# Kernel tuning notes

Hardware: AMD Instinct MI355X
Metric: run time of the kernel (lower is better)

## Reference

```python
import jax, jax.numpy as jnp
from jax import lax
import numpy as np
import math

# --- static equivariant-conv basis (kernel lattice offsets) ---
K = 5          # kernel size = diameter / step
NRB = 3        # num_radial_basis
RMAX = 2.5     # diameter / 2
C0, C1 = 32, 16   # hidden irreps: 32x0e + 16x1e (4*ne scalars + 2*ne vectors, ne=8)
GATES = C1        # one 0e gate scalar per gated vector irrep

_c = np.arange(K, dtype=np.float32) - K // 2
_grid = np.stack(np.meshgrid(_c, _c, _c, indexing='ij'), -1)            # [K,K,K,3]
_norm = np.linalg.norm(_grid, axis=-1)
_mask = (_norm <= RMAX).astype(np.float32)
_ctr = np.linspace(0.0, RMAX, NRB).astype(np.float32)
_w = RMAX / (NRB - 1)
R_BASIS = jnp.asarray(np.exp(-(((_norm[..., None] - _ctr) / _w) ** 2)) * _mask[..., None])  # [K,K,K,NRB]
_safe = np.where(_norm == 0.0, 1.0, _norm)
_y1 = (math.sqrt(3.0) * _grid / _safe[..., None]).astype(np.float32)    # component-normalized l=1 SH
_y1[_norm == 0.0] = 0.0
Y1_SH = jnp.asarray(_y1)                                                # [K,K,K,3]
_levi = np.zeros((3, 3, 3), np.float32)
for _a, _b, _d in ((0, 1, 2), (1, 2, 0), (2, 0, 1)):
    _levi[_a, _b, _d] = 1.0
    _levi[_a, _d, _b] = -1.0
LEVI = jnp.asarray(_levi)


def _equiv_conv(x, ss, sv, vs, vv0, vv1):
    """Equivariant voxel conv: kernel = radial(|r|) * Y_l(r) * CG, then 3D conv.
    x: [B,D,H,W, C0 + 3*C1] -> [B,D,H,W, Cso + 3*Cvo]."""
    Cso, Cvo = ss.shape[-1], sv.shape[-1]
    Kss = jnp.einsum('xyzr,rio->xyzio', R_BASIS, ss)                      # 0e->0e via Y0
    Ksv = jnp.einsum('xyzr,rio,xyzm->xyziom', R_BASIS, sv, Y1_SH)         # 0e->1  via Y1
    Kvs = jnp.einsum('xyzr,rio,xyzm->xyzimo', R_BASIS, vs, Y1_SH) / math.sqrt(3.0)  # 1->0 (dot CG)
    Kvv0 = jnp.einsum('xyzr,rio->xyzio', R_BASIS, vv0)                    # 1->1 via Y0 (identity CG)
    Kvv1 = jnp.einsum('xyzr,rio->xyzio', R_BASIS, vv1)                    # 1->1 via Y1 (cross CG)
    E1 = jnp.einsum('xyzm,amb->xyzab', Y1_SH, LEVI) / math.sqrt(2.0)
    eye = jnp.eye(3, dtype=x.dtype)
    Kvv = (Kvv0[..., :, None, :, None] * eye[None, None, None, None, :, None, :]
           + Kvv1[..., :, None, :, None] * E1[..., None, :, None, :])     # [K,K,K,C1,3,Cvo,3]
    top = jnp.concatenate([Kss, Ksv.reshape(K, K, K, C0, 3 * Cvo)], axis=-1)
    bot = jnp.concatenate([Kvs.reshape(K, K, K, 3 * C1, Cso),
                           Kvv.reshape(K, K, K, 3 * C1, 3 * Cvo)], axis=-1)
    kern = jnp.concatenate([top, bot], axis=-2)                            # [K,K,K,Fin,Fout]
    return lax.conv_general_dilated(x, kern, (1, 1, 1), 'SAME',
                                    dimension_numbers=('NDHWC', 'DHWIO', 'NDHWC'))


def _gate(y):
    """e3nn Gate: activation on scalars, sigmoid(gates) scales the vectors."""
    s = jax.nn.relu(y[..., :C0])
    g = jax.nn.sigmoid(y[..., C0:C0 + GATES])
    v = y[..., C0 + GATES:].reshape(y.shape[:-1] + (C1, 3)) * g[..., None]
    return jnp.concatenate([s, v.reshape(y.shape[:-1] + (3 * C1,))], axis=-1)


def _up2(a, axes=(1, 2, 3)):
    for ax in axes:
        a = jnp.repeat(a, 2, axis=ax)
    return a


def _forward(x, c1_ss, c1_sv, c1_vs, c1_vv0, c1_vv1,
             c2_ss, c2_sv, c2_vs, c2_vv0, c2_vv1, w_pos, wl_s, wl_v):
    # --- ConvolutionBlock: two equivariant convs, each followed by a Gate ---
    x = _gate(_equiv_conv(x, c1_ss, c1_sv, c1_vs, c1_vv0, c1_vv1))
    x = _gate(_equiv_conv(x, c2_ss, c2_sv, c2_vs, c2_vv0, c2_vv1))
    B, Dc, Hc, Wc, _F = x.shape
    # --- _get_vectors: fine-grid offsets to (recentered) upsampled coarse centers ---
    ci = jnp.stack(jnp.meshgrid(jnp.arange(Dc), jnp.arange(Hc), jnp.arange(Wc), indexing='ij'), -1)
    centers = _up2((ci + jnp.array([Dc // 2, Hc // 2, Wc // 2]))[None], (1, 2, 3))[0].astype(jnp.float32)
    fi = jnp.stack(jnp.meshgrid(jnp.arange(2 * Dc), jnp.arange(2 * Hc), jnp.arange(2 * Wc),
                                indexing='ij'), -1).astype(jnp.float32)
    vecs = fi - centers                               # [2D,2H,2W,3]
    p = w_pos * vecs                                  # position_blocks: irreps-wise 1x1 Linear
    # --- nearest-neighbor upsample of features ---
    xu = _up2(x)                                      # [B,2D,2H,2W,F]
    S = xu[..., :C0]
    V = xu[..., C0:].reshape(xu.shape[:-1] + (C1, 3))
    # --- FullTensorProduct(features, pos embedding): per-voxel CG contractions ---
    t_s = jnp.einsum('bxyzcm,xyzm->bxyzc', V, p) / math.sqrt(3.0)          # 1x1->0
    t_v_sp = S[..., None] * p[None, :, :, :, None, :]                       # 0x1->1
    t_v_vp = jnp.cross(V, p[None, :, :, :, None, :]) / math.sqrt(2.0)       # 1x1->1
    tv = jnp.concatenate([t_v_sp, t_v_vp], axis=-2)                         # [...,C0+C1,3]
    # --- rebase_blocks_linear: irreps-wise Linear back to hidden (fan-in normalized) ---
    S_out = jnp.einsum('bxyzc,co->bxyzo', t_s, wl_s) / math.sqrt(C1)
    V_out = jnp.einsum('bxyzcm,co->bxyzom', tv, wl_v) / math.sqrt(C0 + C1)
    return jnp.concatenate([S_out, V_out.reshape(V_out.shape[:-2] + (3 * C1,))], axis=-1)


def setup_inputs() -> dict:
    key = jax.random.key(0)
    ks = jax.random.split(key, 16)
    n = jax.random.normal
    s = 0.02
    B, D = 1, 32
    FIN = C0 + 3 * C1          # 80
    CSO = C0 + GATES           # 48 output scalars (incl. gates) per conv
    return {
        'x': n(ks[0], (B, D, D, D, FIN), jnp.float32),
        'c1_ss': s * n(ks[1], (NRB, C0, CSO), jnp.float32),
        'c1_sv': s * n(ks[2], (NRB, C0, C1), jnp.float32),
        'c1_vs': s * n(ks[3], (NRB, C1, CSO), jnp.float32),
        'c1_vv0': s * n(ks[4], (NRB, C1, C1), jnp.float32),
        'c1_vv1': s * n(ks[5], (NRB, C1, C1), jnp.float32),
        'c2_ss': s * n(ks[6], (NRB, C0, CSO), jnp.float32),
        'c2_sv': s * n(ks[7], (NRB, C0, C1), jnp.float32),
        'c2_vs': s * n(ks[8], (NRB, C1, CSO), jnp.float32),
        'c2_vv0': s * n(ks[9], (NRB, C1, C1), jnp.float32),
        'c2_vv1': s * n(ks[10], (NRB, C1, C1), jnp.float32),
        'w_pos': 0.1 * n(ks[11], (), jnp.float32),
        'wl_s': n(ks[12], (C1, C0), jnp.float32),
        'wl_v': n(ks[13], (C0 + C1, C1), jnp.float32),
    }


def reference(x, c1_ss, c1_sv, c1_vs, c1_vv0, c1_vv1,
              c2_ss, c2_sv, c2_vs, c2_vv0, c2_vv1, w_pos, wl_s, wl_v):
    return _forward(x, c1_ss, c1_sv, c1_vs, c1_vv0, c1_vv1,
                    c2_ss, c2_sv, c2_vs, c2_vv0, c2_vv1, w_pos, wl_s, wl_v)
```

## Files before the change

### kernel.cpp

```cpp
#include <hip/hip_runtime.h>
#include <math.h>


typedef __attribute__((ext_vector_type(8))) short bf16x8;
typedef __attribute__((ext_vector_type(4))) float f32x4;

__device__ __forceinline__ int eps3(int a, int m, int b) {
    if (a == b || a == m || m == b) return 0;
    return ((a==0&&m==1&&b==2)||(a==1&&m==2&&b==0)||(a==2&&m==0&&b==1)) ? 1 : -1;
}

__global__ void build_tap(float* __restrict__ tap) {
    int t = threadIdx.x;
    if (t >= 125) return;
    int td = t / 25 - 2, th = (t / 5) % 5 - 2, tw = t % 5 - 2;
    int n2 = td*td + th*th + tw*tw;
    if (t == 62) {
        float* rec = tap + 40 * 16;
        rec[0] = __int_as_float(0); rec[1] = __int_as_float(0);
        for (int r = 0; r < 3; r++) {
            float tt = (0.f - 1.25f * (float)r) * 0.8f;
            rec[4 + r] = expf(-tt * tt);
        }
        return;
    }
    bool active = n2 <= 6;
    bool pos = (td > 0) || (td == 0 && th > 0) || (td == 0 && th == 0 && tw > 0);
    if (!(active && pos)) return;
    int idx = 0;
    for (int q = 0; q < t; q++) {
        int qd = q / 25 - 2, qh = (q / 5) % 5 - 2, qw = q % 5 - 2;
        int m2 = qd*qd + qh*qh + qw*qw;
        bool p = (qd > 0) || (qd == 0 && qh > 0) || (qd == 0 && qh == 0 && qw > 0);
        if (m2 <= 6 && p) idx++;
    }
    float* rec = tap + idx * 16;
    int off = td * 96 + th * 12 + tw;
    rec[0] = __int_as_float(off);
    rec[1] = __int_as_float(-off);
    float norm = sqrtf((float)n2);
    float comp[3] = {(float)td, (float)th, (float)tw};
    for (int r = 0; r < 3; r++) {
        float tt = (norm - 1.25f * (float)r) * 0.8f;
        float R = expf(-tt * tt);
        rec[4 + r] = R;
        for (int m = 0; m < 3; m++)
            rec[7 + r*3 + m] = R * 1.7320508075688772f * comp[m] / norm;
    }
}

__global__ void build_W(float* __restrict__ W,
    const float* __restrict__ ss1, const float* __restrict__ sv1,
    const float* __restrict__ vs1, const float* __restrict__ vv01, const float* __restrict__ vv11,
    const float* __restrict__ ss2, const float* __restrict__ sv2,
    const float* __restrict__ vs2, const float* __restrict__ vv02, const float* __restrict__ vv12)
{
    int idx = threadIdx.x + blockIdx.x * 256;
    if (idx >= 184320) return;
    int conv = idx / 92160;
    int rem  = idx % 92160;
    int j  = rem / 7680;
    int ci = (rem / 96) % 80;
    int co = rem % 96;
    int r = j >> 2, al = j & 3;
    const float* ss  = conv ? ss2  : ss1;
    const float* sv  = conv ? sv2  : sv1;
    const float* vs  = conv ? vs2  : vs1;
    const float* vv0 = conv ? vv02 : vv01;
    const float* vv1 = conv ? vv12 : vv11;
    float val = 0.f;
    if (ci < 32) {
        if (co < 48) { if (al == 0) val = ss[(r*32 + ci)*48 + co]; }
        else {
            int o = (co - 48) / 3, m = (co - 48) % 3;
            if (al == m + 1) val = sv[(r*32 + ci)*16 + o];
        }
    } else {
        int i = (ci - 32) / 3, a = (ci - 32) % 3;
        if (co < 48) { if (al == a + 1) val = vs[(r*16 + i)*48 + co] * 0.5773502691896258f; }
        else {
            int o = (co - 48) / 3, b = (co - 48) % 3;
            if (al == 0) { if (a == b) val = vv0[(r*16 + i)*16 + o]; }
            else {
                int e = eps3(a, al - 1, b);
                if (e) val = vv1[(r*16 + i)*16 + o] * (float)e * 0.7071067811865476f;
            }
        }
    }
    W[idx] = val;
}

__global__ void build_Wc(const float* __restrict__ W,
                         unsigned short* __restrict__ Wh, unsigned short* __restrict__ Wl)
{
    int idx = threadIdx.x + blockIdx.x * 256;
    if (idx >= 184320) return;
    int conv = idx / 92160, rem = idx % 92160;
    int co = rem / 960, kp = rem % 960;
    int c5 = kp / 192, r2 = kp % 192;
    int j = r2 / 16, ci16 = r2 % 16;
    int k = j * 80 + c5 * 16 + ci16;
    float w = W[conv * 92160 + k * 96 + co];
    unsigned int u = __float_as_uint(w);
    unsigned int hib = (u + 0x7FFFu + ((u >> 16) & 1u)) & 0xFFFF0000u;
    float res = w - __uint_as_float(hib);
    unsigned int v = __float_as_uint(res);
    unsigned int lob = (v + 0x7FFFu + ((v >> 16) & 1u)) >> 16;
    Wh[idx] = (unsigned short)(hib >> 16);
    Wl[idx] = (unsigned short)lob;
}

__device__ __forceinline__ void split8(float4 a, float4 b, bf16x8& hi, bf16x8& lo) {
    float av[8] = {a.x, a.y, a.z, a.w, b.x, b.y, b.z, b.w};
    #pragma unroll
    for (int e = 0; e < 8; e++) {
        unsigned int u = __float_as_uint(av[e]);
        hi[e] = (short)(u >> 16);
        float res = av[e] - __uint_as_float(u & 0xFFFF0000u);
        lo[e] = (short)(__float_as_uint(res) >> 16);
    }
}

__global__ __launch_bounds__(512, 2) void fused_conv(
    const float* __restrict__ xin, const unsigned short* __restrict__ Wh,
    const unsigned short* __restrict__ Wl, const float* __restrict__ tap,
    float* __restrict__ xout)
{
    __shared__ float smem[38400];
    int tid = threadIdx.x;
    int cl = tid >> 7;
    int vl = tid & 127;
    int dl = vl >> 5, hl = (vl >> 3) & 3, wl = vl & 7;
    int w8 = tid >> 6, l = tid & 63;
    int lr = l & 15, lk = l >> 4;
    int bid = blockIdx.x;
    int dt = (bid >> 5) << 2;
    int h0 = ((bid >> 2) & 7) << 2;
    int w0 = (bid & 3) << 3;

    int gof[6];
    int lof[6];
    #pragma unroll
    for (int q = 0; q < 6; q++) {
        int i = tid + q * 512;
        int sl = i / 768, rr = i - sl * 768;
        int dd = rr / 96, rm = rr - dd * 96;
        int hh = rm / 12, ww = rm - hh * 12;
        int gd = dt + dd - 2, gh = h0 + hh - 2, gw = w0 + ww - 2;
        gof[q] = (gd >= 0 && gd < 32 && gh >= 0 && gh < 32 && gw >= 0 && gw < 32)
               ? (((gd << 5) + gh) * 32 + gw) * 80 + sl * 4 : -1;
        lof[q] = sl * 3072 + rr * 4;
    }

    {
        float4 pf[6];
        #pragma unroll
        for (int q = 0; q < 6; q++)
            pf[q] = (gof[q] >= 0) ? *reinterpret_cast<const float4*>(xin + gof[q])
                                  : make_float4(0.f, 0.f, 0.f, 0.f);
        #pragma unroll
        for (int q = 0; q < 6; q++)
            *reinterpret_cast<float4*>(smem + lof[q]) = pf[q];
    }
    __syncthreads();

    const f32x4 fzero = {0.f, 0.f, 0.f, 0.f};
    f32x4 acc[6];
    #pragma unroll
    for (int nt = 0; nt < 6; nt++) acc[nt] = fzero;

    float* zcb = smem + 12288;
    const float* xp = smem + cl * 3072 + (((dl + 2) * 8 + hl + 2) * 12 + (wl + 2)) * 4;
    float* zp = zcb + vl * 204;

    for (int c5 = 0; c5 < 5; c5++) {
        float4 pf[6];
        if (c5 < 4) {
            int chof = (c5 + 1) * 16;
            #pragma unroll
            for (int q = 0; q < 6; q++)
                pf[q] = (gof[q] >= 0) ? *reinterpret_cast<const float4*>(xin + gof[q] + chof)
                                      : make_float4(0.f, 0.f, 0.f, 0.f);
        }
        {
            float az[12][4];
            #pragma unroll
            for (int j = 0; j < 12; j++)
                #pragma unroll
                for (int c = 0; c < 4; c++) az[j][c] = 0.f;
            {
                const float* rec = tap + 640;
                float4 xc = *reinterpret_cast<const float4*>(xp);
                #pragma unroll
                for (int r = 0; r < 3; r++) {
                    float R = rec[4 + r];
                    az[r*4][0] += R * xc.x; az[r*4][1] += R * xc.y;
                    az[r*4][2] += R * xc.z; az[r*4][3] += R * xc.w;
                }
            }
            for (int p = 0; p < 40; p++) {
                const float* rec = tap + p * 16;
                int op = __float_as_int(rec[0]) * 4, om = __float_as_int(rec[1]) * 4;
                float4 xa = *reinterpret_cast<const float4*>(xp + op);
                float4 xb = *reinterpret_cast<const float4*>(xp + om);
                float s[4], d[4];
                s[0] = xa.x + xb.x; s[1] = xa.y + xb.y; s[2] = xa.z + xb.z; s[3] = xa.w + xb.w;
                d[0] = xa.x - xb.x; d[1] = xa.y - xb.y; d[2] = xa.z - xb.z; d[3] = xa.w - xb.w;
                #pragma unroll
                for (int r = 0; r < 3; r++) {
                    float R = rec[4 + r];
                    #pragma unroll
                    for (int c = 0; c < 4; c++) az[r*4][c] += R * s[c];
                    #pragma unroll
                    for (int m = 0; m < 3; m++) {
                        float RY = rec[7 + r*3 + m];
                        #pragma unroll
                        for (int c = 0; c < 4; c++) az[r*4 + m + 1][c] += RY * d[c];
                    }
                }
            }
            #pragma unroll
            for (int j = 0; j < 12; j++)
                *reinterpret_cast<float4*>(zp + j * 16 + cl * 4) =
                    make_float4(az[j][0], az[j][1], az[j][2], az[j][3]);
        }
        __syncthreads();
        if (c5 < 4) {
            #pragma unroll
            for (int q = 0; q < 6; q++)
                *reinterpret_cast<float4*>(smem + lof[q]) = pf[q];
        }
        const float* ap0 = zcb + (w8 * 16 + lr) * 204 + lk * 8;
        #pragma unroll
        for (int ks = 0; ks < 6; ks++) {
            const unsigned short* bbh = Wh + lr * 960 + c5 * 192 + ks * 32 + lk * 8;
            const unsigned short* bbl = Wl + lr * 960 + c5 * 192 + ks * 32 + lk * 8;
            bf16x8 bh[6], bl[6];
            #pragma unroll
            for (int nt = 0; nt < 6; nt++) {
                bh[nt] = *reinterpret_cast<const bf16x8*>(bbh + nt * 15360);
                bl[nt] = *reinterpret_cast<const bf16x8*>(bbl + nt * 15360);
            }
            const float* ap = ap0 + ks * 32;
            bf16x8 ah, al;
            split8(*reinterpret_cast<const float4*>(ap),
                   *reinterpret_cast<const float4*>(ap + 4), ah, al);
            #pragma unroll
            for (int nt = 0; nt < 6; nt++) {
                acc[nt] = __builtin_amdgcn_mfma_f32_16x16x32_bf16(ah, bh[nt], acc[nt], 0, 0, 0);
                acc[nt] = __builtin_amdgcn_mfma_f32_16x16x32_bf16(al, bh[nt], acc[nt], 0, 0, 0);
                acc[nt] = __builtin_amdgcn_mfma_f32_16x16x32_bf16(ah, bl[nt], acc[nt], 0, 0, 0);
            }
        }
        __syncthreads();
    }

    float* y = smem;
    #pragma unroll
    for (int nt = 0; nt < 6; nt++)
        #pragma unroll
        for (int r = 0; r < 4; r++)
            y[(w8 * 16 + lk * 4 + r) * 98 + nt * 16 + lr] = acc[nt][r];
    __syncthreads();
    #pragma unroll
    for (int it = 0; it < 20; it++) {
        int idx = tid + it * 512;
        int vr = idx / 80, c = idx - vr * 80;
        int gd = dt + (vr >> 5), gh = h0 + ((vr >> 3) & 3), gw = w0 + (vr & 7);
        const float* yr = y + vr * 98;
        float val;
        if (c < 32) val = fmaxf(yr[c], 0.f);
        else {
            int q = c - 32;
            float g = 1.f / (1.f + __expf(-yr[32 + q / 3]));
            val = yr[48 + q] * g;
        }
        xout[(size_t)(((gd << 5) + gh) * 32 + gw) * 80 + c] = val;
    }
}

__global__ __launch_bounds__(256) void final_k(
    const float* __restrict__ x2, const float* __restrict__ wls,
    const float* __restrict__ wlv, const float* __restrict__ wpos,
    float* __restrict__ out)
{
    __shared__ float xv[16 * 81];
    __shared__ float coeff[16 * 161];
    __shared__ float s_wls[512];
    __shared__ float s_wlv[768];
    int t = threadIdx.x;
    int bid = blockIdx.x;
    int cw0 = (bid & 1) * 16;
    int ch  = (bid >> 1) & 31;
    int cd  = bid >> 6;
    float wp = wpos[0];
    {
        int base = ((cd * 32 + ch) * 32 + cw0) * 80;
        #pragma unroll
        for (int i = t; i < 1280; i += 256) {
            int vi = i / 80, c = i % 80;
            xv[vi * 81 + c] = x2[base + i];
        }
        for (int i = t; i < 512; i += 256) s_wls[i] = wls[i];
        for (int i = t; i < 768; i += 256) s_wlv[i] = wlv[i];
    }
    __syncthreads();
    {
        int vi = t >> 4, j = t & 15;
        const float* xp = xv + vi * 81;
        float* cf = coeff + vi * 161;
        #pragma unroll
        for (int l = 0; l < 10; l++) {
            int q = l * 16 + j;
            float sum = 0.f;
            if (q < 96) {
                int o = q / 3, m = q % 3;
                #pragma unroll
                for (int c = 0; c < 16; c++) sum += xp[32 + c * 3 + m] * s_wls[c * 32 + o];
            } else if (q < 112) {
                int o = q - 96;
                #pragma unroll
                for (int c = 0; c < 32; c++) sum += xp[c] * s_wlv[c * 16 + o];
            } else {
                int q2 = q - 112; int o = q2 / 3, m = q2 % 3;
                #pragma unroll
                for (int c = 0; c < 16; c++) sum += xp[32 + c * 3 + m] * s_wlv[(32 + c) * 16 + o];
            }
            cf[q] = sum;
        }
    }
    __syncthreads();
    const float scale = 0.14433756729740643f;
    #pragma unroll
    for (int f01 = 0; f01 < 4; f01++) {
        int fd = 2 * cd + (f01 >> 1), fh = 2 * ch + (f01 & 1);
        float p0 = wp * (float)(cd + (f01 >> 1) - 16);
        float p1 = wp * (float)(ch + (f01 & 1) - 16);
        size_t obase = (size_t)((fd * 64 + fh) * 64 + cw0 * 2) * 80;
        #pragma unroll
        for (int it = 0; it < 10; it++) {
            int idx = it * 256 + t;
            int fwl = idx / 80, c = idx - fwl * 80;
            int vi = fwl >> 1;
            float p2 = wp * (float)(cw0 + vi + (fwl & 1) - 16);
            const float* cf = coeff + vi * 161;
            float val;
            if (c < 32) {
                val = cf[c * 3] * p0 + cf[c * 3 + 1] * p1 + cf[c * 3 + 2] * p2;
            } else {
                int q = c - 32, o = q / 3, m = q - o * 3;
                float A = cf[96 + o];
                const float* w2 = cf + 112 + o * 3;
                float pm, crm;
                if (m == 0)      { pm = p0; crm = w2[1] * p2 - w2[2] * p1; }
                else if (m == 1) { pm = p1; crm = w2[2] * p0 - w2[0] * p2; }
                else             { pm = p2; crm = w2[0] * p1 - w2[1] * p0; }
                val = A * pm + crm * 0.7071067811865476f;
            }
            out[obase + idx] = val * scale;
        }
    }
}

extern "C" void kernel_launch(void* const* d_in, const int* in_sizes, int n_in,
                              void* d_out, int out_size, void* d_ws, size_t ws_size,
                              hipStream_t stream)
{
    const float* x    = (const float*)d_in[0];
    const float* wpos = (const float*)d_in[11];
    const float* wls  = (const float*)d_in[12];
    const float* wlv  = (const float*)d_in[13];
    float* out = (float*)d_out;
    float* ws  = (float*)d_ws;

    float* tap = ws;
    float* W   = ws + 1024;
    unsigned short* Wh = (unsigned short*)(ws + 1024 + 184320);
    unsigned short* Wl = Wh + 184320;
    float* x1  = ws + 1024 + 184320 + 184320;
    float* x2  = x1 + 2621440;

    build_tap<<<1, 128, 0, stream>>>(tap);
    build_W<<<720, 256, 0, stream>>>(W,
        (const float*)d_in[1], (const float*)d_in[2], (const float*)d_in[3],
        (const float*)d_in[4], (const float*)d_in[5],
        (const float*)d_in[6], (const float*)d_in[7], (const float*)d_in[8],
        (const float*)d_in[9], (const float*)d_in[10]);
    build_Wc<<<720, 256, 0, stream>>>(W, Wh, Wl);

    fused_conv<<<256, 512, 0, stream>>>(x,  Wh,         Wl,         tap, x1);
    fused_conv<<<256, 512, 0, stream>>>(x1, Wh + 92160, Wl + 92160, tap, x2);
    final_k<<<2048, 256, 0, stream>>>(x2, wls, wlv, wpos, out);
}
```

Baseline: 419.9 us.

## Double fused_conv block size to 1024 threads and vectorize final_k stores

```diff
diff --git a/kernel.cpp b/kernel.cpp
--- a/kernel.cpp
+++ b/kernel.cpp
@@ -121,28 +121,27 @@
     }
 }
 
-__global__ __launch_bounds__(512, 2) void fused_conv(
+__global__ __launch_bounds__(1024, 4) void fused_conv(
     const float* __restrict__ xin, const unsigned short* __restrict__ Wh,
     const unsigned short* __restrict__ Wl, const float* __restrict__ tap,
     float* __restrict__ xout)
 {
-    __shared__ float smem[38400];
+    __shared__ float smem[37376];
     int tid = threadIdx.x;
-    int cl = tid >> 7;
-    int vl = tid & 127;
+    int vl = tid & 127, cg = tid >> 7;
     int dl = vl >> 5, hl = (vl >> 3) & 3, wl = vl & 7;
-    int w8 = tid >> 6, l = tid & 63;
+    int w16 = tid >> 6, l = tid & 63;
     int lr = l & 15, lk = l >> 4;
+    int rt = w16 >> 1, nh = w16 & 1;
     int bid = blockIdx.x;
     int dt = (bid >> 5) << 2;
     int h0 = ((bid >> 2) & 7) << 2;
     int w0 = (bid & 3) << 3;
 
-    int gof[6];
-    int lof[6];
-    #pragma unroll
-    for (int q = 0; q < 6; q++) {
-        int i = tid + q * 512;
+    int gof[3], lof[3];
+    #pragma unroll
+    for (int q = 0; q < 3; q++) {
+        int i = tid + q * 1024;
         int sl = i / 768, rr = i - sl * 768;
         int dd = rr / 96, rm = rr - dd * 96;
         int hh = rm / 12, ww = rm - hh * 12;
@@ -153,92 +152,86 @@
     }
 
     {
-        float4 pf[6];
-        #pragma unroll
-        for (int q = 0; q < 6; q++)
+        float4 pf[3];
+        #pragma unroll
+        for (int q = 0; q < 3; q++)
             pf[q] = (gof[q] >= 0) ? *reinterpret_cast<const float4*>(xin + gof[q])
                                   : make_float4(0.f, 0.f, 0.f, 0.f);
         #pragma unroll
-        for (int q = 0; q < 6; q++)
+        for (int q = 0; q < 3; q++)
             *reinterpret_cast<float4*>(smem + lof[q]) = pf[q];
     }
     __syncthreads();
 
     const f32x4 fzero = {0.f, 0.f, 0.f, 0.f};
-    f32x4 acc[6];
-    #pragma unroll
-    for (int nt = 0; nt < 6; nt++) acc[nt] = fzero;
-
-    float* zcb = smem + 12288;
-    const float* xp = smem + cl * 3072 + (((dl + 2) * 8 + hl + 2) * 12 + (wl + 2)) * 4;
-    float* zp = zcb + vl * 204;
+    f32x4 acc[3];
+    #pragma unroll
+    for (int nt = 0; nt < 3; nt++) acc[nt] = fzero;
+
+    const float* xp = smem + (cg >> 1) * 3072
+                    + (((dl + 2) * 8 + hl + 2) * 12 + (wl + 2)) * 4 + (cg & 1) * 2;
+    float* zp = smem + 12288 + vl * 196 + cg * 2;
+    const float* ap0 = smem + 12288 + (rt * 16 + lr) * 196 + lk * 8;
 
     for (int c5 = 0; c5 < 5; c5++) {
-        float4 pf[6];
+        float4 pf[3];
         if (c5 < 4) {
             int chof = (c5 + 1) * 16;
             #pragma unroll
-            for (int q = 0; q < 6; q++)
+            for (int q = 0; q < 3; q++)
                 pf[q] = (gof[q] >= 0) ? *reinterpret_cast<const float4*>(xin + gof[q] + chof)
                                       : make_float4(0.f, 0.f, 0.f, 0.f);
         }
         {
-            float az[12][4];
-            #pragma unroll
-            for (int j = 0; j < 12; j++)
-                #pragma unroll
-                for (int c = 0; c < 4; c++) az[j][c] = 0.f;
+            float az[12][2];
+            #pragma unroll
+            for (int j = 0; j < 12; j++) { az[j][0] = 0.f; az[j][1] = 0.f; }
             {
                 const float* rec = tap + 640;
-                float4 xc = *reinterpret_cast<const float4*>(xp);
+                float2 xc = *reinterpret_cast<const float2*>(xp);
                 #pragma unroll
                 for (int r = 0; r < 3; r++) {
                     float R = rec[4 + r];
                     az[r*4][0] += R * xc.x; az[r*4][1] += R * xc.y;
-                    az[r*4][2] += R * xc.z; az[r*4][3] += R * xc.w;
                 }
             }
             for (int p = 0; p < 40; p++) {
                 const float* rec = tap + p * 16;
                 int op = __float_as_int(rec[0]) * 4, om = __float_as_int(rec[1]) * 4;
-                float4 xa = *reinterpret_cast<const float4*>(xp + op);
-                float4 xb = *reinterpret_cast<const float4*>(xp + om);
-                float s[4], d[4];
-                s[0] = xa.x + xb.x; s[1] = xa.y + xb.y; s[2] = xa.z + xb.z; s[3] = xa.w + xb.w;
-                d[0] = xa.x - xb.x; d[1] = xa.y - xb.y; d[2] = xa.z - xb.z; d[3] = xa.w - xb.w;
+                float2 xa = *reinterpret_cast<const float2*>(xp + op);
+                float2 xb = *reinterpret_cast<const float2*>(xp + om);
+                float s0 = xa.x + xb.x, s1 = xa.y + xb.y;
+                float d0 = xa.x - xb.x, d1 = xa.y - xb.y;
                 #pragma unroll
                 for (int r = 0; r < 3; r++) {
                     float R = rec[4 + r];
-                    #pragma unroll
-                    for (int c = 0; c < 4; c++) az[r*4][c] += R * s[c];
+                    az[r*4][0] += R * s0; az[r*4][1] += R * s1;
                     #pragma unroll
                     for (int m = 0; m < 3; m++) {
                         float RY = rec[7 + r*3 + m];
-                        #pragma unroll
-                        for (int c = 0; c < 4; c++) az[r*4 + m + 1][c] += RY * d[c];
+                        az[r*4 + m + 1][0] += RY * d0;
+                        az[r*4 + m + 1][1] += RY * d1;
                     }
                 }
             }
             #pragma unroll
             for (int j = 0; j < 12; j++)
-                *reinterpret_cast<float4*>(zp + j * 16 + cl * 4) =
-                    make_float4(az[j][0], az[j][1], az[j][2], az[j][3]);
+                *reinterpret_cast<float2*>(zp + j * 16) = make_float2(az[j][0], az[j][1]);
         }
         __syncthreads();
         if (c5 < 4) {
             #pragma unroll
-            for (int q = 0; q < 6; q++)
+            for (int q = 0; q < 3; q++)
                 *reinterpret_cast<float4*>(smem + lof[q]) = pf[q];
         }
-        const float* ap0 = zcb + (w8 * 16 + lr) * 204 + lk * 8;
         #pragma unroll
         for (int ks = 0; ks < 6; ks++) {
-            const unsigned short* bbh = Wh + lr * 960 + c5 * 192 + ks * 32 + lk * 8;
-            const unsigned short* bbl = Wl + lr * 960 + c5 * 192 + ks * 32 + lk * 8;
-            bf16x8 bh[6], bl[6];
-            #pragma unroll
-            for (int nt = 0; nt < 6; nt++) {
-                bh[nt] = *reinterpret_cast<const bf16x8*>(bbh + nt * 15360);
+            const unsigned short* bb = Wh + (nh * 48 + lr) * 960 + c5 * 192 + ks * 32 + lk * 8;
+            const unsigned short* bbl = Wl + (nh * 48 + lr) * 960 + c5 * 192 + ks * 32 + lk * 8;
+            bf16x8 bh[3], bl[3];
+            #pragma unroll
+            for (int nt = 0; nt < 3; nt++) {
+                bh[nt] = *reinterpret_cast<const bf16x8*>(bb  + nt * 15360);
                 bl[nt] = *reinterpret_cast<const bf16x8*>(bbl + nt * 15360);
             }
             const float* ap = ap0 + ks * 32;
@@ -246,7 +239,7 @@
             split8(*reinterpret_cast<const float4*>(ap),
                    *reinterpret_cast<const float4*>(ap + 4), ah, al);
             #pragma unroll
-            for (int nt = 0; nt < 6; nt++) {
+            for (int nt = 0; nt < 3; nt++) {
                 acc[nt] = __builtin_amdgcn_mfma_f32_16x16x32_bf16(ah, bh[nt], acc[nt], 0, 0, 0);
                 acc[nt] = __builtin_amdgcn_mfma_f32_16x16x32_bf16(al, bh[nt], acc[nt], 0, 0, 0);
                 acc[nt] = __builtin_amdgcn_mfma_f32_16x16x32_bf16(ah, bl[nt], acc[nt], 0, 0, 0);
@@ -257,14 +250,14 @@
 
     float* y = smem;
     #pragma unroll
-    for (int nt = 0; nt < 6; nt++)
+    for (int nt = 0; nt < 3; nt++)
         #pragma unroll
         for (int r = 0; r < 4; r++)
-            y[(w8 * 16 + lk * 4 + r) * 98 + nt * 16 + lr] = acc[nt][r];
+            y[(rt * 16 + lk * 4 + r) * 98 + nh * 48 + nt * 16 + lr] = acc[nt][r];
     __syncthreads();
     #pragma unroll
-    for (int it = 0; it < 20; it++) {
-        int idx = tid + it * 512;
+    for (int it = 0; it < 10; it++) {
+        int idx = tid + it * 1024;
         int vr = idx / 80, c = idx - vr * 80;
         int gd = dt + (vr >> 5), gh = h0 + ((vr >> 3) & 3), gw = w0 + (vr & 7);
         const float* yr = y + vr * 98;
@@ -338,26 +331,37 @@
         float p1 = wp * (float)(ch + (f01 & 1) - 16);
         size_t obase = (size_t)((fd * 64 + fh) * 64 + cw0 * 2) * 80;
         #pragma unroll
-        for (int it = 0; it < 10; it++) {
-            int idx = it * 256 + t;
-            int fwl = idx / 80, c = idx - fwl * 80;
-            int vi = fwl >> 1;
-            float p2 = wp * (float)(cw0 + vi + (fwl & 1) - 16);
-            const float* cf = coeff + vi * 161;
-            float val;
-            if (c < 32) {
-                val = cf[c * 3] * p0 + cf[c * 3 + 1] * p1 + cf[c * 3 + 2] * p2;
-            } else {
-                int q = c - 32, o = q / 3, m = q - o * 3;
-                float A = cf[96 + o];
-                const float* w2 = cf + 112 + o * 3;
-                float pm, crm;
-                if (m == 0)      { pm = p0; crm = w2[1] * p2 - w2[2] * p1; }
-                else if (m == 1) { pm = p1; crm = w2[2] * p0 - w2[0] * p2; }
-                else             { pm = p2; crm = w2[0] * p1 - w2[1] * p0; }
-                val = A * pm + crm * 0.7071067811865476f;
-            }
-            out[obase + idx] = val * scale;
+        for (int it = 0; it < 3; it++) {
+            int idx4 = it * 256 + t;
+            if (idx4 < 640) {
+                int base = idx4 * 4;
+                int fwl = base / 80, c0 = base - fwl * 80;
+                int vi = fwl >> 1;
+                float p2 = wp * (float)(cw0 + vi + (fwl & 1) - 16);
+                const float* cf = coeff + vi * 161;
+                float vv[4];
+                if (c0 < 32) {
+                    #pragma unroll
+                    for (int e = 0; e < 4; e++) {
+                        int c = c0 + e;
+                        vv[e] = cf[c * 3] * p0 + cf[c * 3 + 1] * p1 + cf[c * 3 + 2] * p2;
+                    }
+                } else {
+                    #pragma unroll
+                    for (int e = 0; e < 4; e++) {
+                        int q = c0 - 32 + e, o = q / 3, m = q - o * 3;
+                        float A = cf[96 + o];
+                        const float* w2 = cf + 112 + o * 3;
+                        float pm, crm;
+                        if (m == 0)      { pm = p0; crm = w2[1] * p2 - w2[2] * p1; }
+                        else if (m == 1) { pm = p1; crm = w2[2] * p0 - w2[0] * p2; }
+                        else             { pm = p2; crm = w2[0] * p1 - w2[1] * p0; }
+                        vv[e] = A * pm + crm * 0.7071067811865476f;
+                    }
+                }
+                *reinterpret_cast<float4*>(out + obase + base) =
+                    make_float4(vv[0]*scale, vv[1]*scale, vv[2]*scale, vv[3]*scale);
+            }
         }
     }
 }
@@ -388,7 +392,7 @@
         (const float*)d_in[9], (const float*)d_in[10]);
     build_Wc<<<720, 256, 0, stream>>>(W, Wh, Wl);
 
-    fused_conv<<<256, 512, 0, stream>>>(x,  Wh,         Wl,         tap, x1);
-    fused_conv<<<256, 512, 0, stream>>>(x1, Wh + 92160, Wl + 92160, tap, x2);
+    fused_conv<<<256, 1024, 0, stream>>>(x,  Wh,         Wl,         tap, x1);
+    fused_conv<<<256, 1024, 0, stream>>>(x1, Wh + 92160, Wl + 92160, tap, x2);
     final_k<<<2048, 256, 0, stream>>>(x2, wls, wlv, wpos, out);
 }
```

Measured after the change: 411.3 us. 2.0% less time.
